# Performance work log

Measured on AMD Instinct MI355X. Metric: run time of the kernel, lower is better.

## Reference

```python
import jax
import jax.numpy as jnp
from jax import lax
import numpy as np

N, D, V, T = 16384, 256, 32000, 128
U_DECAY = 0.97


def _ln_row(z, eps=1e-6):
    # torch layernorm_row: (z - mean) / (std_unbiased + eps)
    m = z.mean(axis=-1, keepdims=True)
    s = z.std(axis=-1, ddof=1, keepdims=True)  # torch .std is unbiased
    return (z - m) / (s + eps)


def setup_inputs() -> dict:
    key = jax.random.key(0)
    k0, k1, k2, k3, k4 = jax.random.split(key, 5)
    E = jax.random.normal(k0, (D, N), dtype=jnp.float32) / np.sqrt(N).astype(np.float32)
    Dx = jax.random.normal(k1, (N, D), dtype=jnp.float32) / np.sqrt(D).astype(np.float32)
    Dy = jax.random.normal(k2, (N, D), dtype=jnp.float32) / np.sqrt(D).astype(np.float32)
    token_emb = jax.random.normal(k3, (V, D), dtype=jnp.float32) / np.sqrt(D).astype(np.float32)
    tokens = jax.random.randint(k4, (T,), 0, V)
    return {"E": E, "Dx": Dx, "Dy": Dy, "token_emb": token_emb, "tokens": tokens}


def reference(E, Dx, Dy, token_emb, tokens):
    d, n = E.shape

    def step(carry, tok):
        x, rho = carry
        v_prev = token_emb[tok]                    # [d]
        x_t = x + jax.nn.relu(Dx @ v_prev)         # [n], use_relu_lowrank=True
        a_star = rho @ x_t                         # [d]
        y_core = Dy @ _ln_row(a_star)              # [n], ln_before_Dy=True
        y_t = jax.nn.relu(y_core) * jnp.maximum(x_t, 0.0)
        v_star = _ln_row(E @ y_t)                  # [d]
        rho = U_DECAY * (rho + jnp.outer(v_prev, x_t))  # rank-1 write + decay
        return (x_t, rho), (y_t, v_star)

    x0 = jnp.zeros((n,), dtype=E.dtype)
    rho0 = jnp.zeros((d, n), dtype=E.dtype)
    (x_f, rho_f), (ys, vs) = lax.scan(step, (x0, rho0), tokens)
    # final states x, y, v, rho concatenated into one vector
    return jnp.concatenate([x_f, ys[-1], vs[-1], rho_f.ravel()])
```

## Files before the change

kernel.cpp:

```cpp
#include <hip/hip_runtime.h>
#include <cstddef>

namespace {
constexpr int Nn = 16384;
constexpr int Dd = 256;
constexpr int Tt = 128;
constexpr float DECAY = 0.97f;

constexpr size_t WS_V    = 0;
constexpr size_t WS_CUMV = WS_V + (size_t)Tt * Dd;
constexpr size_t WS_M    = WS_CUMV + (size_t)Tt * Dd;
constexpr size_t WS_H    = WS_M + (size_t)Nn * Tt;
constexpr size_t WS_LNA  = WS_H + Tt;
constexpr size_t WS_U    = WS_LNA + Dd;
}

__global__ void k_gather(const float* __restrict__ temb, const int* __restrict__ toks,
                         float* __restrict__ Vb, float* __restrict__ h) {
  int t = blockIdx.x;
  int d = threadIdx.x;
  Vb[t * Dd + d] = temb[(size_t)toks[t] * Dd + d];
  if (blockIdx.x == 0 && threadIdx.x < Tt) h[threadIdx.x] = 0.f;
}

__global__ void k_cumv(const float* __restrict__ Vb, float* __restrict__ cumV) {
  int d = threadIdx.x;
  float run = 0.f, w = DECAY;
  for (int t = Tt - 1; t >= 0; --t) {
    run += w * Vb[t * Dd + d];
    cumV[t * Dd + d] = run;
    w *= DECAY;
  }
}

__global__ __launch_bounds__(256) void k_gemm_M(const float* __restrict__ Dx,
                                                const float* __restrict__ Vb,
                                                float* __restrict__ M,
                                                float* __restrict__ xf) {
  __shared__ __align__(16) float As[32 * 64];
  __shared__ __align__(16) float Bs[32 * 128];
  const int tid = threadIdx.x;
  const int tx = tid & 15, ty = tid >> 4;
  const int j0 = blockIdx.x * 64;
  float acc[4][8] = {};
  const float4* Dx4 = (const float4*)Dx;
  const float4* Vb4 = (const float4*)Vb;

  for (int ch = 0; ch < 8; ++ch) {
    __syncthreads();
#pragma unroll
    for (int i = 0; i < 2; ++i) {
      int idx = tid + i * 256;
      int row = idx >> 3, k4 = idx & 7;
      float4 v = Dx4[(size_t)(j0 + row) * 64 + ch * 8 + k4];
      As[(k4 * 4 + 0) * 64 + row] = v.x;
      As[(k4 * 4 + 1) * 64 + row] = v.y;
      As[(k4 * 4 + 2) * 64 + row] = v.z;
      As[(k4 * 4 + 3) * 64 + row] = v.w;
    }
#pragma unroll
    for (int i = 0; i < 4; ++i) {
      int idx = tid + i * 256;
      int t = idx >> 3, k4 = idx & 7;
      float4 v = Vb4[(size_t)t * 64 + ch * 8 + k4];
      Bs[(k4 * 4 + 0) * 128 + t] = v.x;
      Bs[(k4 * 4 + 1) * 128 + t] = v.y;
      Bs[(k4 * 4 + 2) * 128 + t] = v.z;
      Bs[(k4 * 4 + 3) * 128 + t] = v.w;
    }
    __syncthreads();
#pragma unroll
    for (int kk = 0; kk < 32; ++kk) {
      float4 a = *(const float4*)&As[kk * 64 + ty * 4];
      float4 b0 = *(const float4*)&Bs[kk * 128 + tx * 8];
      float4 b1 = *(const float4*)&Bs[kk * 128 + tx * 8 + 4];
      float av[4] = {a.x, a.y, a.z, a.w};
      float bv[8] = {b0.x, b0.y, b0.z, b0.w, b1.x, b1.y, b1.z, b1.w};
#pragma unroll
      for (int r = 0; r < 4; ++r)
#pragma unroll
        for (int c = 0; c < 8; ++c) acc[r][c] += av[r] * bv[c];
    }
  }
  float rs[4];
#pragma unroll
  for (int r = 0; r < 4; ++r) {
    float s = 0.f;
#pragma unroll
    for (int c = 0; c < 8; ++c) {
      acc[r][c] = fmaxf(acc[r][c], 0.f);
      s += acc[r][c];
    }
    rs[r] = s;
    int j = j0 + ty * 4 + r;
    float4 o0 = {acc[r][0], acc[r][1], acc[r][2], acc[r][3]};
    float4 o1 = {acc[r][4], acc[r][5], acc[r][6], acc[r][7]};
    *(float4*)&M[(size_t)j * Tt + tx * 8] = o0;
    *(float4*)&M[(size_t)j * Tt + tx * 8 + 4] = o1;
  }
  __syncthreads();
  float* red = As;
#pragma unroll
  for (int r = 0; r < 4; ++r) red[(ty * 4 + r) * 17 + tx] = rs[r];
  __syncthreads();
  if (tid < 64) {
    float s = 0.f;
#pragma unroll
    for (int x = 0; x < 16; ++x) s += red[tid * 17 + x];
    xf[j0 + tid] = s;
  }
}

__global__ void k_h(const float* __restrict__ M, const float* __restrict__ x,
                    float* __restrict__ h) {
  __shared__ float red[256];
  const int tid = threadIdx.x;
  const int s = tid & 127, half = tid >> 7;
  const int jbase = blockIdx.x * 64 + half * 32;
  float acc = 0.f;
  for (int i = 0; i < 32; ++i) {
    int j = jbase + i;
    acc += M[(size_t)j * Tt + s] * x[j];
  }
  red[tid] = acc;
  __syncthreads();
  if (tid < 128) atomicAdd(&h[tid], red[tid] + red[tid + 128]);
}

__global__ void k_astar(const float* __restrict__ h, const float* __restrict__ Vb,
                        float* __restrict__ lna) {
  __shared__ float g[Tt];
  __shared__ float red[256];
  const int d = threadIdx.x;
  if (d == 0) {
    float run = 0.f;
    for (int t = 0; t < Tt; ++t) {
      run += h[t];
      g[t] = run;
    }
  }
  __syncthreads();
  float a = 0.f, w = DECAY;
  for (int t = Tt - 2; t >= 0; --t) {
    a += w * g[t] * Vb[t * Dd + d];
    w *= DECAY;
  }
  red[d] = a;
  __syncthreads();
  for (int off = 128; off > 0; off >>= 1) {
    if (d < off) red[d] += red[d + off];
    __syncthreads();
  }
  float m = red[0] * (1.f / 256.f);
  __syncthreads();
  float c = a - m;
  red[d] = c * c;
  __syncthreads();
  for (int off = 128; off > 0; off >>= 1) {
    if (d < off) red[d] += red[d + off];
    __syncthreads();
  }
  float sd = sqrtf(red[0] * (1.f / 255.f));
  lna[d] = c / (sd + 1e-6f);
}

__global__ void k_y(const float* __restrict__ Dy, const float* __restrict__ lna,
                    const float* __restrict__ x, float* __restrict__ yout) {
  const int tid = threadIdx.x;
  const int wave = tid >> 6, lane = tid & 63;
  const int j = blockIdx.x * 4 + wave;
  const float4* Dy4 = (const float4*)Dy;
  const float4* l4 = (const float4*)lna;
  float4 a = Dy4[(size_t)j * 64 + lane];
  float4 b = l4[lane];
  float acc = a.x * b.x + a.y * b.y + a.z * b.z + a.w * b.w;
#pragma unroll
  for (int off = 32; off > 0; off >>= 1) acc += __shfl_down(acc, off);
  if (lane == 0) {
    yout[j] = fmaxf(acc, 0.f) * fmaxf(x[j], 0.f);
  }
}

__global__ void k_u(const float* __restrict__ E, const float* __restrict__ y,
                    float* __restrict__ u) {
  __shared__ float red[256];
  const int d = blockIdx.x, tid = threadIdx.x;
  const float4* E4 = (const float4*)E;
  const float4* y4 = (const float4*)y;
  float acc = 0.f;
  for (int i = 0; i < 16; ++i) {
    int idx = tid + i * 256;
    float4 e = E4[(size_t)d * 4096 + idx];
    float4 yv = y4[idx];
    acc += e.x * yv.x + e.y * yv.y + e.z * yv.z + e.w * yv.w;
  }
  red[tid] = acc;
  __syncthreads();
  for (int off = 128; off > 0; off >>= 1) {
    if (tid < off) red[tid] += red[tid + off];
    __syncthreads();
  }
  if (tid == 0) u[d] = red[0];
}

__global__ void k_ln_u(const float* __restrict__ u, float* __restrict__ vout) {
  __shared__ float red[256];
  const int d = threadIdx.x;
  float a = u[d];
  red[d] = a;
  __syncthreads();
  for (int off = 128; off > 0; off >>= 1) {
    if (d < off) red[d] += red[d + off];
    __syncthreads();
  }
  float m = red[0] * (1.f / 256.f);
  __syncthreads();
  float c = a - m;
  red[d] = c * c;
  __syncthreads();
  for (int off = 128; off > 0; off >>= 1) {
    if (d < off) red[d] += red[d + off];
    __syncthreads();
  }
  float sd = sqrtf(red[0] * (1.f / 255.f));
  vout[d] = c / (sd + 1e-6f);
}

__global__ __launch_bounds__(256) void k_rho(const float* __restrict__ cumV,
                                             const float* __restrict__ M,
                                             float* __restrict__ rho) {
  __shared__ __align__(16) float As[32 * 64];
  __shared__ __align__(16) float Bs[32 * 128];
  const int tid = threadIdx.x;
  const int tx = tid & 15, ty = tid >> 4;
  const int d0 = (blockIdx.x & 3) * 64;
  const int j0 = (blockIdx.x >> 2) * 128;
  float acc[4][8] = {};
  const float4* C4 = (const float4*)cumV;
  const float4* M4 = (const float4*)M;

  for (int ch = 0; ch < 4; ++ch) {
    __syncthreads();
#pragma unroll
    for (int i = 0; i < 2; ++i) {
      int idx = tid + i * 256;
      int k = idx >> 4, d4 = idx & 15;
      float4 v = C4[(size_t)(ch * 32 + k) * 64 + (d0 >> 2) + d4];
      *(float4*)&As[k * 64 + d4 * 4] = v;
    }
#pragma unroll
    for (int i = 0; i < 4; ++i) {
      int idx = tid + i * 256;
      int j = idx >> 3, k4 = idx & 7;
      float4 v = M4[(size_t)(j0 + j) * 32 + ch * 8 + k4];
      Bs[(k4 * 4 + 0) * 128 + j] = v.x;
      Bs[(k4 * 4 + 1) * 128 + j] = v.y;
      Bs[(k4 * 4 + 2) * 128 + j] = v.z;
      Bs[(k4 * 4 + 3) * 128 + j] = v.w;
    }
    __syncthreads();
#pragma unroll
    for (int kk = 0; kk < 32; ++kk) {
      float4 a = *(const float4*)&As[kk * 64 + ty * 4];
      float4 b0 = *(const float4*)&Bs[kk * 128 + tx * 8];
      float4 b1 = *(const float4*)&Bs[kk * 128 + tx * 8 + 4];
      float av[4] = {a.x, a.y, a.z, a.w};
      float bv[8] = {b0.x, b0.y, b0.z, b0.w, b1.x, b1.y, b1.z, b1.w};
#pragma unroll
      for (int r = 0; r < 4; ++r)
#pragma unroll
        for (int c = 0; c < 8; ++c) acc[r][c] += av[r] * bv[c];
    }
  }
#pragma unroll
  for (int r = 0; r < 4; ++r) {
    int d = d0 + ty * 4 + r;
    float4 o0 = {acc[r][0], acc[r][1], acc[r][2], acc[r][3]};
    float4 o1 = {acc[r][4], acc[r][5], acc[r][6], acc[r][7]};
    *(float4*)&rho[(size_t)d * Nn + j0 + tx * 8] = o0;
    *(float4*)&rho[(size_t)d * Nn + j0 + tx * 8 + 4] = o1;
  }
}

extern "C" void kernel_launch(void* const* d_in, const int* in_sizes, int n_in,
                              void* d_out, int out_size, void* d_ws, size_t ws_size,
                              hipStream_t stream) {
  const float* E = (const float*)d_in[0];
  const float* Dx = (const float*)d_in[1];
  const float* Dy = (const float*)d_in[2];
  const float* temb = (const float*)d_in[3];
  const int* toks = (const int*)d_in[4];

  float* out = (float*)d_out;
  float* ws = (float*)d_ws;
  float* Vb   = ws + WS_V;
  float* cumV = ws + WS_CUMV;
  float* M    = ws + WS_M;
  float* h    = ws + WS_H;
  float* lna  = ws + WS_LNA;
  float* u    = ws + WS_U;

  float* xf  = out;
  float* yv  = out + Nn;
  float* vs  = out + 2 * Nn;
  float* rho = out + 2 * Nn + Dd;

  k_gather<<<Tt, Dd, 0, stream>>>(temb, toks, Vb, h);
  k_cumv<<<1, Dd, 0, stream>>>(Vb, cumV);
  k_gemm_M<<<Nn / 64, 256, 0, stream>>>(Dx, Vb, M, xf);
  k_h<<<Nn / 64, 256, 0, stream>>>(M, xf, h);
  k_astar<<<1, Dd, 0, stream>>>(h, Vb, lna);
  k_y<<<Nn / 4, 256, 0, stream>>>(Dy, lna, xf, yv);
  k_u<<<Dd, 256, 0, stream>>>(E, yv, u);
  k_ln_u<<<1, Dd, 0, stream>>>(u, vs);
  k_rho<<<(Nn / 128) * 4, 256, 0, stream>>>(cumV, M, rho);
}
```

Before: 187.8 us.

## Fuse all stages into one persistent kernel with software grid barriers

Replaces the nine separate launches with one persistent 256-block kernel that uses atomic-counter grid barriers between the dependent phases. The h reduction is folded into the M GEMM epilogue, and Dy@lna, E@y and rho are computed by the same blocks. Register prefetch double-buffers the GEMM loads, and the token-embedding gather is done directly instead of through a staging buffer. This removes launch gaps and intermediate global round-trips, but relies on all 256 blocks being co-resident and leaves only 256 blocks for the rho GEMM, where the old code launched 512.

New measurement: 393.5 us. 109% more time.

```diff
diff --git a/kernel.cpp b/kernel.cpp
--- a/kernel.cpp
+++ b/kernel.cpp
@@ -6,279 +6,325 @@
 constexpr int Dd = 256;
 constexpr int Tt = 128;
 constexpr float DECAY = 0.97f;
-
-constexpr size_t WS_V    = 0;
-constexpr size_t WS_CUMV = WS_V + (size_t)Tt * Dd;
-constexpr size_t WS_M    = WS_CUMV + (size_t)Tt * Dd;
-constexpr size_t WS_H    = WS_M + (size_t)Nn * Tt;
-constexpr size_t WS_LNA  = WS_H + Tt;
-constexpr size_t WS_U    = WS_LNA + Dd;
+constexpr int NB = 256;
+constexpr int TPB = 256;
+
+constexpr size_t WS_M    = 0;
+constexpr size_t WS_CUMV = WS_M + (size_t)Nn * Tt;
+constexpr size_t WS_H    = WS_CUMV + (size_t)Tt * Dd;
+constexpr size_t WS_U    = WS_H + Tt;
+constexpr size_t WS_BAR  = WS_U + Dd;
 }
 
-__global__ void k_gather(const float* __restrict__ temb, const int* __restrict__ toks,
-                         float* __restrict__ Vb, float* __restrict__ h) {
-  int t = blockIdx.x;
-  int d = threadIdx.x;
-  Vb[t * Dd + d] = temb[(size_t)toks[t] * Dd + d];
-  if (blockIdx.x == 0 && threadIdx.x < Tt) h[threadIdx.x] = 0.f;
+__device__ __forceinline__ void grid_barrier(unsigned* cnt, unsigned* gen) {
+  __syncthreads();
+  if (threadIdx.x == 0) {
+    unsigned g = __hip_atomic_load(gen, __ATOMIC_RELAXED, __HIP_MEMORY_SCOPE_AGENT);
+    __threadfence();
+    unsigned old = __hip_atomic_fetch_add(cnt, 1u, __ATOMIC_ACQ_REL, __HIP_MEMORY_SCOPE_AGENT);
+    if (old == NB - 1) {
+      __hip_atomic_store(cnt, 0u, __ATOMIC_RELAXED, __HIP_MEMORY_SCOPE_AGENT);
+      __hip_atomic_store(gen, g + 1u, __ATOMIC_RELEASE, __HIP_MEMORY_SCOPE_AGENT);
+    } else {
+      while (__hip_atomic_load(gen, __ATOMIC_ACQUIRE, __HIP_MEMORY_SCOPE_AGENT) == g)
+        __builtin_amdgcn_s_sleep(8);
+    }
+    __threadfence();
+  }
+  __syncthreads();
 }
 
-__global__ void k_cumv(const float* __restrict__ Vb, float* __restrict__ cumV) {
-  int d = threadIdx.x;
-  float run = 0.f, w = DECAY;
-  for (int t = Tt - 1; t >= 0; --t) {
-    run += w * Vb[t * Dd + d];
-    cumV[t * Dd + d] = run;
-    w *= DECAY;
-  }
-}
-
-__global__ __launch_bounds__(256) void k_gemm_M(const float* __restrict__ Dx,
-                                                const float* __restrict__ Vb,
-                                                float* __restrict__ M,
-                                                float* __restrict__ xf) {
-  __shared__ __align__(16) float As[32 * 64];
-  __shared__ __align__(16) float Bs[32 * 128];
+__global__ __launch_bounds__(TPB) void k_fused(
+    const float* __restrict__ E, const float* __restrict__ Dx,
+    const float* __restrict__ Dy, const float* __restrict__ temb,
+    const int* __restrict__ toks, float* __restrict__ ws,
+    float* __restrict__ out) {
+  float* Mg   = ws + WS_M;
+  float* cumV = ws + WS_CUMV;
+  float* h    = ws + WS_H;
+  float* u    = ws + WS_U;
+  unsigned* bar = (unsigned*)(ws + WS_BAR);
+
+  float* xf  = out;
+  float* yv  = out + Nn;
+  float* vs  = out + 2 * Nn;
+  float* rho = out + 2 * Nn + Dd;
+
+  __shared__ __align__(16) float smem[32 * 64 + 32 * 128];
+  float* As = smem;
+  float* Bs = smem + 32 * 64;
+  __shared__ float xjl[64];
+  __shared__ int s_toks[Tt];
+  __shared__ float g_l[Tt];
+  __shared__ float red_l[Dd];
+  __shared__ float lna_l[Dd];
+  __shared__ float y_l[64];
+
   const int tid = threadIdx.x;
+  const int b = blockIdx.x;
   const int tx = tid & 15, ty = tid >> 4;
-  const int j0 = blockIdx.x * 64;
-  float acc[4][8] = {};
-  const float4* Dx4 = (const float4*)Dx;
-  const float4* Vb4 = (const float4*)Vb;
-
-  for (int ch = 0; ch < 8; ++ch) {
-    __syncthreads();
-#pragma unroll
-    for (int i = 0; i < 2; ++i) {
-      int idx = tid + i * 256;
-      int row = idx >> 3, k4 = idx & 7;
-      float4 v = Dx4[(size_t)(j0 + row) * 64 + ch * 8 + k4];
-      As[(k4 * 4 + 0) * 64 + row] = v.x;
-      As[(k4 * 4 + 1) * 64 + row] = v.y;
-      As[(k4 * 4 + 2) * 64 + row] = v.z;
-      As[(k4 * 4 + 3) * 64 + row] = v.w;
-    }
-#pragma unroll
-    for (int i = 0; i < 4; ++i) {
-      int idx = tid + i * 256;
-      int t = idx >> 3, k4 = idx & 7;
-      float4 v = Vb4[(size_t)t * 64 + ch * 8 + k4];
-      Bs[(k4 * 4 + 0) * 128 + t] = v.x;
-      Bs[(k4 * 4 + 1) * 128 + t] = v.y;
-      Bs[(k4 * 4 + 2) * 128 + t] = v.z;
-      Bs[(k4 * 4 + 3) * 128 + t] = v.w;
-    }
-    __syncthreads();
-#pragma unroll
-    for (int kk = 0; kk < 32; ++kk) {
-      float4 a = *(const float4*)&As[kk * 64 + ty * 4];
-      float4 b0 = *(const float4*)&Bs[kk * 128 + tx * 8];
-      float4 b1 = *(const float4*)&Bs[kk * 128 + tx * 8 + 4];
-      float av[4] = {a.x, a.y, a.z, a.w};
-      float bv[8] = {b0.x, b0.y, b0.z, b0.w, b1.x, b1.y, b1.z, b1.w};
-#pragma unroll
-      for (int r = 0; r < 4; ++r)
-#pragma unroll
-        for (int c = 0; c < 8; ++c) acc[r][c] += av[r] * bv[c];
-    }
-  }
-  float rs[4];
-#pragma unroll
-  for (int r = 0; r < 4; ++r) {
-    float s = 0.f;
+  const int lane = tid & 63, wv = tid >> 6;
+
+  if (tid < Tt) s_toks[tid] = toks[tid];
+  __syncthreads();
+
+  if (b < Tt) {
+    const int s = b;
+    float run = 0.f, w = DECAY;
+    for (int t = Tt - 1; t >= s; --t) {
+      run += w * temb[(size_t)s_toks[t] * Dd + tid];
+      w *= DECAY;
+    }
+    cumV[s * Dd + tid] = run;
+  }
+
+  {
+    const int j0 = b * 64;
+    const float4* Dx4 = (const float4*)Dx;
+    const float4* T4 = (const float4*)temb;
+    float acc[4][8] = {};
+    float4 pa[2], pb[4];
+    auto loadA = [&](int ch, int i) {
+      int idx = tid + i * 256, row = idx >> 3, k4 = idx & 7;
+      return Dx4[(size_t)(j0 + row) * 64 + ch * 8 + k4];
+    };
+    auto loadB = [&](int ch, int i) {
+      int idx = tid + i * 256, t = idx >> 3, k4 = idx & 7;
+      return T4[(size_t)s_toks[t] * 64 + ch * 8 + k4];
+    };
+    pa[0] = loadA(0, 0); pa[1] = loadA(0, 1);
+    pb[0] = loadB(0, 0); pb[1] = loadB(0, 1);
+    pb[2] = loadB(0, 2); pb[3] = loadB(0, 3);
+
+    for (int ch = 0; ch < 8; ++ch) {
+      __syncthreads();
+#pragma unroll
+      for (int i = 0; i < 2; ++i) {
+        int idx = tid + i * 256, row = idx >> 3, k4 = idx & 7;
+        As[(k4 * 4 + 0) * 64 + row] = pa[i].x;
+        As[(k4 * 4 + 1) * 64 + row] = pa[i].y;
+        As[(k4 * 4 + 2) * 64 + row] = pa[i].z;
+        As[(k4 * 4 + 3) * 64 + row] = pa[i].w;
+      }
+#pragma unroll
+      for (int i = 0; i < 4; ++i) {
+        int idx = tid + i * 256, t = idx >> 3, k4 = idx & 7;
+        Bs[(k4 * 4 + 0) * 128 + t] = pb[i].x;
+        Bs[(k4 * 4 + 1) * 128 + t] = pb[i].y;
+        Bs[(k4 * 4 + 2) * 128 + t] = pb[i].z;
+        Bs[(k4 * 4 + 3) * 128 + t] = pb[i].w;
+      }
+      __syncthreads();
+      if (ch < 7) {
+        pa[0] = loadA(ch + 1, 0); pa[1] = loadA(ch + 1, 1);
+        pb[0] = loadB(ch + 1, 0); pb[1] = loadB(ch + 1, 1);
+        pb[2] = loadB(ch + 1, 2); pb[3] = loadB(ch + 1, 3);
+      }
+#pragma unroll
+      for (int kk = 0; kk < 32; ++kk) {
+        float4 a = *(const float4*)&As[kk * 64 + ty * 4];
+        float4 b0 = *(const float4*)&Bs[kk * 128 + tx * 8];
+        float4 b1 = *(const float4*)&Bs[kk * 128 + tx * 8 + 4];
+        float avv[4] = {a.x, a.y, a.z, a.w};
+        float bvv[8] = {b0.x, b0.y, b0.z, b0.w, b1.x, b1.y, b1.z, b1.w};
+#pragma unroll
+        for (int r = 0; r < 4; ++r)
+#pragma unroll
+          for (int c = 0; c < 8; ++c) acc[r][c] += avv[r] * bvv[c];
+      }
+    }
+    float rs[4];
+#pragma unroll
+    for (int r = 0; r < 4; ++r) {
+      float s = 0.f;
+#pragma unroll
+      for (int c = 0; c < 8; ++c) {
+        acc[r][c] = fmaxf(acc[r][c], 0.f);
+        s += acc[r][c];
+      }
+      rs[r] = s;
+      int j = j0 + ty * 4 + r;
+      float4 o0 = {acc[r][0], acc[r][1], acc[r][2], acc[r][3]};
+      float4 o1 = {acc[r][4], acc[r][5], acc[r][6], acc[r][7]};
+      *(float4*)&Mg[(size_t)j * Tt + tx * 8] = o0;
+      *(float4*)&Mg[(size_t)j * Tt + tx * 8 + 4] = o1;
+    }
+    __syncthreads();
+    float* redx = As;
+#pragma unroll
+    for (int r = 0; r < 4; ++r) redx[(ty * 4 + r) * 17 + tx] = rs[r];
+    __syncthreads();
+    if (tid < 64) {
+      float s = 0.f;
+#pragma unroll
+      for (int x = 0; x < 16; ++x) s += redx[tid * 17 + x];
+      xjl[tid] = s;
+      xf[j0 + tid] = s;
+    }
+    __syncthreads();
+    float* hred = Bs;
 #pragma unroll
     for (int c = 0; c < 8; ++c) {
-      acc[r][c] = fmaxf(acc[r][c], 0.f);
-      s += acc[r][c];
-    }
-    rs[r] = s;
-    int j = j0 + ty * 4 + r;
-    float4 o0 = {acc[r][0], acc[r][1], acc[r][2], acc[r][3]};
-    float4 o1 = {acc[r][4], acc[r][5], acc[r][6], acc[r][7]};
-    *(float4*)&M[(size_t)j * Tt + tx * 8] = o0;
-    *(float4*)&M[(size_t)j * Tt + tx * 8 + 4] = o1;
-  }
-  __syncthreads();
-  float* red = As;
-#pragma unroll
-  for (int r = 0; r < 4; ++r) red[(ty * 4 + r) * 17 + tx] = rs[r];
-  __syncthreads();
-  if (tid < 64) {
-    float s = 0.f;
-#pragma unroll
-    for (int x = 0; x < 16; ++x) s += red[tid * 17 + x];
-    xf[j0 + tid] = s;
-  }
-}
-
-__global__ void k_h(const float* __restrict__ M, const float* __restrict__ x,
-                    float* __restrict__ h) {
-  __shared__ float red[256];
-  const int tid = threadIdx.x;
-  const int s = tid & 127, half = tid >> 7;
-  const int jbase = blockIdx.x * 64 + half * 32;
-  float acc = 0.f;
-  for (int i = 0; i < 32; ++i) {
-    int j = jbase + i;
-    acc += M[(size_t)j * Tt + s] * x[j];
-  }
-  red[tid] = acc;
-  __syncthreads();
-  if (tid < 128) atomicAdd(&h[tid], red[tid] + red[tid + 128]);
-}
-
-__global__ void k_astar(const float* __restrict__ h, const float* __restrict__ Vb,
-                        float* __restrict__ lna) {
-  __shared__ float g[Tt];
-  __shared__ float red[256];
-  const int d = threadIdx.x;
-  if (d == 0) {
-    float run = 0.f;
-    for (int t = 0; t < Tt; ++t) {
-      run += h[t];
-      g[t] = run;
-    }
-  }
-  __syncthreads();
-  float a = 0.f, w = DECAY;
-  for (int t = Tt - 2; t >= 0; --t) {
-    a += w * g[t] * Vb[t * Dd + d];
-    w *= DECAY;
-  }
-  red[d] = a;
-  __syncthreads();
-  for (int off = 128; off > 0; off >>= 1) {
-    if (d < off) red[d] += red[d + off];
-    __syncthreads();
-  }
-  float m = red[0] * (1.f / 256.f);
-  __syncthreads();
-  float c = a - m;
-  red[d] = c * c;
-  __syncthreads();
-  for (int off = 128; off > 0; off >>= 1) {
-    if (d < off) red[d] += red[d + off];
-    __syncthreads();
-  }
-  float sd = sqrtf(red[0] * (1.f / 255.f));
-  lna[d] = c / (sd + 1e-6f);
-}
-
-__global__ void k_y(const float* __restrict__ Dy, const float* __restrict__ lna,
-                    const float* __restrict__ x, float* __restrict__ yout) {
-  const int tid = threadIdx.x;
-  const int wave = tid >> 6, lane = tid & 63;
-  const int j = blockIdx.x * 4 + wave;
-  const float4* Dy4 = (const float4*)Dy;
-  const float4* l4 = (const float4*)lna;
-  float4 a = Dy4[(size_t)j * 64 + lane];
-  float4 b = l4[lane];
-  float acc = a.x * b.x + a.y * b.y + a.z * b.z + a.w * b.w;
-#pragma unroll
-  for (int off = 32; off > 0; off >>= 1) acc += __shfl_down(acc, off);
-  if (lane == 0) {
-    yout[j] = fmaxf(acc, 0.f) * fmaxf(x[j], 0.f);
-  }
-}
-
-__global__ void k_u(const float* __restrict__ E, const float* __restrict__ y,
-                    float* __restrict__ u) {
-  __shared__ float red[256];
-  const int d = blockIdx.x, tid = threadIdx.x;
-  const float4* E4 = (const float4*)E;
-  const float4* y4 = (const float4*)y;
-  float acc = 0.f;
-  for (int i = 0; i < 16; ++i) {
-    int idx = tid + i * 256;
-    float4 e = E4[(size_t)d * 4096 + idx];
-    float4 yv = y4[idx];
-    acc += e.x * yv.x + e.y * yv.y + e.z * yv.z + e.w * yv.w;
-  }
-  red[tid] = acc;
-  __syncthreads();
-  for (int off = 128; off > 0; off >>= 1) {
-    if (tid < off) red[tid] += red[tid + off];
-    __syncthreads();
-  }
-  if (tid == 0) u[d] = red[0];
-}
-
-__global__ void k_ln_u(const float* __restrict__ u, float* __restrict__ vout) {
-  __shared__ float red[256];
-  const int d = threadIdx.x;
-  float a = u[d];
-  red[d] = a;
-  __syncthreads();
-  for (int off = 128; off > 0; off >>= 1) {
-    if (d < off) red[d] += red[d + off];
-    __syncthreads();
-  }
-  float m = red[0] * (1.f / 256.f);
-  __syncthreads();
-  float c = a - m;
-  red[d] = c * c;
-  __syncthreads();
-  for (int off = 128; off > 0; off >>= 1) {
-    if (d < off) red[d] += red[d + off];
-    __syncthreads();
-  }
-  float sd = sqrtf(red[0] * (1.f / 255.f));
-  vout[d] = c / (sd + 1e-6f);
-}
-
-__global__ __launch_bounds__(256) void k_rho(const float* __restrict__ cumV,
-                                             const float* __restrict__ M,
-                                             float* __restrict__ rho) {
-  __shared__ __align__(16) float As[32 * 64];
-  __shared__ __align__(16) float Bs[32 * 128];
-  const int tid = threadIdx.x;
-  const int tx = tid & 15, ty = tid >> 4;
-  const int d0 = (blockIdx.x & 3) * 64;
-  const int j0 = (blockIdx.x >> 2) * 128;
-  float acc[4][8] = {};
-  const float4* C4 = (const float4*)cumV;
-  const float4* M4 = (const float4*)M;
-
-  for (int ch = 0; ch < 4; ++ch) {
-    __syncthreads();
-#pragma unroll
-    for (int i = 0; i < 2; ++i) {
-      int idx = tid + i * 256;
-      int k = idx >> 4, d4 = idx & 15;
-      float4 v = C4[(size_t)(ch * 32 + k) * 64 + (d0 >> 2) + d4];
-      *(float4*)&As[k * 64 + d4 * 4] = v;
-    }
-#pragma unroll
-    for (int i = 0; i < 4; ++i) {
-      int idx = tid + i * 256;
-      int j = idx >> 3, k4 = idx & 7;
-      float4 v = M4[(size_t)(j0 + j) * 32 + ch * 8 + k4];
-      Bs[(k4 * 4 + 0) * 128 + j] = v.x;
-      Bs[(k4 * 4 + 1) * 128 + j] = v.y;
-      Bs[(k4 * 4 + 2) * 128 + j] = v.z;
-      Bs[(k4 * 4 + 3) * 128 + j] = v.w;
-    }
-    __syncthreads();
-#pragma unroll
-    for (int kk = 0; kk < 32; ++kk) {
-      float4 a = *(const float4*)&As[kk * 64 + ty * 4];
-      float4 b0 = *(const float4*)&Bs[kk * 128 + tx * 8];
-      float4 b1 = *(const float4*)&Bs[kk * 128 + tx * 8 + 4];
-      float av[4] = {a.x, a.y, a.z, a.w};
-      float bv[8] = {b0.x, b0.y, b0.z, b0.w, b1.x, b1.y, b1.z, b1.w};
-#pragma unroll
-      for (int r = 0; r < 4; ++r)
-#pragma unroll
-        for (int c = 0; c < 8; ++c) acc[r][c] += av[r] * bv[c];
-    }
-  }
-#pragma unroll
-  for (int r = 0; r < 4; ++r) {
-    int d = d0 + ty * 4 + r;
-    float4 o0 = {acc[r][0], acc[r][1], acc[r][2], acc[r][3]};
-    float4 o1 = {acc[r][4], acc[r][5], acc[r][6], acc[r][7]};
-    *(float4*)&rho[(size_t)d * Nn + j0 + tx * 8] = o0;
-    *(float4*)&rho[(size_t)d * Nn + j0 + tx * 8 + 4] = o1;
+      float p = 0.f;
+#pragma unroll
+      for (int r = 0; r < 4; ++r) p += acc[r][c] * xjl[ty * 4 + r];
+      hred[(tx * 8 + c) * 17 + ty] = p;
+    }
+    __syncthreads();
+    if (tid < Tt) {
+      float s = 0.f;
+#pragma unroll
+      for (int i = 0; i < 16; ++i) s += hred[tid * 17 + i];
+      atomicAdd(&h[tid], s);
+    }
+  }
+
+  grid_barrier(&bar[0], &bar[1]);
+
+  {
+    if (tid < Tt) g_l[tid] = h[tid];
+    __syncthreads();
+    if (tid == 0) {
+      float run = 0.f;
+      for (int t = 0; t < Tt; ++t) { run += g_l[t]; g_l[t] = run; }
+    }
+    __syncthreads();
+    float a = 0.f, w = DECAY;
+    for (int t = Tt - 2; t >= 0; --t) {
+      a += w * g_l[t] * temb[(size_t)s_toks[t] * Dd + tid];
+      w *= DECAY;
+    }
+    red_l[tid] = a;
+    __syncthreads();
+    for (int off = 128; off > 0; off >>= 1) {
+      if (tid < off) red_l[tid] += red_l[tid + off];
+      __syncthreads();
+    }
+    float m = red_l[0] * (1.f / 256.f);
+    __syncthreads();
+    float c0 = a - m;
+    red_l[tid] = c0 * c0;
+    __syncthreads();
+    for (int off = 128; off > 0; off >>= 1) {
+      if (tid < off) red_l[tid] += red_l[tid + off];
+      __syncthreads();
+    }
+    float sd = sqrtf(red_l[0] * (1.f / 255.f));
+    lna_l[tid] = c0 / (sd + 1e-6f);
+    __syncthreads();
+
+    const int j0 = b * 64;
+    const float4* Dy4 = (const float4*)Dy;
+    const float4* l4 = (const float4*)lna_l;
+    for (int i = 0; i < 16; ++i) {
+      int jl = wv * 16 + i, j = j0 + jl;
+      float4 dv = Dy4[(size_t)j * 64 + lane];
+      float4 lv = l4[lane];
+      float accy = dv.x * lv.x + dv.y * lv.y + dv.z * lv.z + dv.w * lv.w;
+#pragma unroll
+      for (int off = 32; off > 0; off >>= 1) accy += __shfl_down(accy, off);
+      if (lane == 0) {
+        float yy = fmaxf(accy, 0.f) * fmaxf(xjl[jl], 0.f);
+        y_l[jl] = yy;
+        yv[j] = yy;
+      }
+    }
+    __syncthreads();
+    float yj = y_l[lane];
+    for (int i = 0; i < 64; ++i) {
+      int d = wv * 64 + i;
+      float p = E[(size_t)d * Nn + j0 + lane] * yj;
+#pragma unroll
+      for (int off = 32; off > 0; off >>= 1) p += __shfl_down(p, off);
+      if (lane == 0) atomicAdd(&u[d], p);
+    }
+  }
+
+  grid_barrier(&bar[0], &bar[1]);
+
+  if (b == 0) {
+    float a = u[tid];
+    red_l[tid] = a;
+    __syncthreads();
+    for (int off = 128; off > 0; off >>= 1) {
+      if (tid < off) red_l[tid] += red_l[tid + off];
+      __syncthreads();
+    }
+    float m = red_l[0] * (1.f / 256.f);
+    __syncthreads();
+    float c0 = a - m;
+    red_l[tid] = c0 * c0;
+    __syncthreads();
+    for (int off = 128; off > 0; off >>= 1) {
+      if (tid < off) red_l[tid] += red_l[tid + off];
+      __syncthreads();
+    }
+    float sd = sqrtf(red_l[0] * (1.f / 255.f));
+    vs[tid] = c0 / (sd + 1e-6f);
+  }
+
+  {
+    const float4* C4 = (const float4*)cumV;
+    const float4* M4 = (const float4*)Mg;
+    for (int tt = 2 * b; tt <= 2 * b + 1; ++tt) {
+      const int d0 = (tt & 3) * 64;
+      const int j0r = (tt >> 2) * 128;
+      float acc[4][8] = {};
+      float4 qa[2], qb[4];
+      auto loadRA = [&](int ch, int i) {
+        int idx = tid + i * 256, k = idx >> 4, d4 = idx & 15;
+        return C4[(size_t)(ch * 32 + k) * 64 + (d0 >> 2) + d4];
+      };
+      auto loadRB = [&](int ch, int i) {
+        int idx = tid + i * 256, j = idx >> 3, k4 = idx & 7;
+        return M4[(size_t)(j0r + j) * 32 + ch * 8 + k4];
+      };
+      qa[0] = loadRA(0, 0); qa[1] = loadRA(0, 1);
+      qb[0] = loadRB(0, 0); qb[1] = loadRB(0, 1);
+      qb[2] = loadRB(0, 2); qb[3] = loadRB(0, 3);
+      for (int ch = 0; ch < 4; ++ch) {
+        __syncthreads();
+#pragma unroll
+        for (int i = 0; i < 2; ++i) {
+          int idx = tid + i * 256, k = idx >> 4, d4 = idx & 15;
+          *(float4*)&As[k * 64 + d4 * 4] = qa[i];
+        }
+#pragma unroll
+        for (int i = 0; i < 4; ++i) {
+          int idx = tid + i * 256, j = idx >> 3, k4 = idx & 7;
+          Bs[(k4 * 4 + 0) * 128 + j] = qb[i].x;
+          Bs[(k4 * 4 + 1) * 128 + j] = qb[i].y;
+          Bs[(k4 * 4 + 2) * 128 + j] = qb[i].z;
+          Bs[(k4 * 4 + 3) * 128 + j] = qb[i].w;
+        }
+        __syncthreads();
+        if (ch < 3) {
+          qa[0] = loadRA(ch + 1, 0); qa[1] = loadRA(ch + 1, 1);
+          qb[0] = loadRB(ch + 1, 0); qb[1] = loadRB(ch + 1, 1);
+          qb[2] = loadRB(ch + 1, 2); qb[3] = loadRB(ch + 1, 3);
+        }
+#pragma unroll
+        for (int kk = 0; kk < 32; ++kk) {
+          float4 a = *(const float4*)&As[kk * 64 + ty * 4];
+          float4 b0 = *(const float4*)&Bs[kk * 128 + tx * 8];
+          float4 b1 = *(const float4*)&Bs[kk * 128 + tx * 8 + 4];
+          float avv[4] = {a.x, a.y, a.z, a.w};
+          float bvv[8] = {b0.x, b0.y, b0.z, b0.w, b1.x, b1.y, b1.z, b1.w};
+#pragma unroll
+          for (int r = 0; r < 4; ++r)
+#pragma unroll
+            for (int c = 0; c < 8; ++c) acc[r][c] += avv[r] * bvv[c];
+        }
+      }
+#pragma unroll
+      for (int r = 0; r < 4; ++r) {
+        int d = d0 + ty * 4 + r;
+        float4 o0 = {acc[r][0], acc[r][1], acc[r][2], acc[r][3]};
+        float4 o1 = {acc[r][4], acc[r][5], acc[r][6], acc[r][7]};
+        *(float4*)&rho[(size_t)d * Nn + j0r + tx * 8] = o0;
+        *(float4*)&rho[(size_t)d * Nn + j0r + tx * 8 + 4] = o1;
+      }
+    }
   }
 }
 
@@ -291,27 +337,10 @@
   const float* temb = (const float*)d_in[3];
   const int* toks = (const int*)d_in[4];
 
+  float* ws = (float*)d_ws;
   float* out = (float*)d_out;
-  float* ws = (float*)d_ws;
-  float* Vb   = ws + WS_V;
-  float* cumV = ws + WS_CUMV;
-  float* M    = ws + WS_M;
-  float* h    = ws + WS_H;
-  float* lna  = ws + WS_LNA;
-  float* u    = ws + WS_U;
-
-  float* xf  = out;
-  float* yv  = out + Nn;
-  float* vs  = out + 2 * Nn;
-  float* rho = out + 2 * Nn + Dd;
-
-  k_gather<<<Tt, Dd, 0, stream>>>(temb, toks, Vb, h);
-  k_cumv<<<1, Dd, 0, stream>>>(Vb, cumV);
-  k_gemm_M<<<Nn / 64, 256, 0, stream>>>(Dx, Vb, M, xf);
-  k_h<<<Nn / 64, 256, 0, stream>>>(M, xf, h);
-  k_astar<<<1, Dd, 0, stream>>>(h, Vb, lna);
-  k_y<<<Nn / 4, 256, 0, stream>>>(Dy, lna, xf, yv);
-  k_u<<<Dd, 256, 0, stream>>>(E, yv, u);
-  k_ln_u<<<1, Dd, 0, stream>>>(u, vs);
-  k_rho<<<(Nn / 128) * 4, 256, 0, stream>>>(cumV, M, rho);
+
+  hipMemsetAsync(ws + WS_H, 0, (Tt + Dd + 8) * sizeof(float), stream);
+
+  k_fused<<<NB, TPB, 0, stream>>>(E, Dx, Dy, temb, toks, ws, out);
 }
```
